# Performance work log

Measured on AMD Instinct MI355X. Metric: run time of the kernel, lower is better.

Reference implementation:

```python
import jax, jax.numpy as jnp
import numpy as np

B, H, W, DIM = 16, 64, 64, 512
GH, GW = 8, 8
NH = 16
HD = DIM // NH
POS = DIM // 16  # DynamicPosBias pos_dim = (dim//4)//4 = 32
EPS = 1e-5


def setup_inputs() -> dict:
    key = jax.random.key(0)
    ks = jax.random.split(key, 12)
    w = lambda k, s: jax.random.normal(k, s, jnp.float32) * 0.02
    f32 = jnp.float32
    return {
        "x": jax.random.normal(ks[0], (B, H * W, DIM), f32),
        "norm1_g": jnp.ones((DIM,), f32), "norm1_b": jnp.zeros((DIM,), f32),
        "qkv_w": w(ks[1], (3 * DIM, DIM)), "qkv_b": jnp.zeros((3 * DIM,), f32),
        "proj_w": w(ks[2], (DIM, DIM)), "proj_b": jnp.zeros((DIM,), f32),
        "pos_w0": w(ks[3], (POS, 2)), "pos_b0": jnp.zeros((POS,), f32),
        "pos_ln0_g": jnp.ones((POS,), f32), "pos_ln0_b": jnp.zeros((POS,), f32),
        "pos_w1": w(ks[4], (POS, POS)), "pos_b1": jnp.zeros((POS,), f32),
        "pos_ln1_g": jnp.ones((POS,), f32), "pos_ln1_b": jnp.zeros((POS,), f32),
        "pos_w2": w(ks[5], (POS, POS)), "pos_b2": jnp.zeros((POS,), f32),
        "pos_ln2_g": jnp.ones((POS,), f32), "pos_ln2_b": jnp.zeros((POS,), f32),
        "pos_w3": w(ks[6], (NH, POS)), "pos_b3": jnp.zeros((NH,), f32),
        "norm2_g": jnp.ones((DIM,), f32), "norm2_b": jnp.zeros((DIM,), f32),
        "mlp_w1": w(ks[7], (4 * DIM, DIM)), "mlp_b1": jnp.zeros((4 * DIM,), f32),
        "mlp_w2": w(ks[8], (DIM, 4 * DIM)), "mlp_b2": jnp.zeros((DIM,), f32),
    }


def _ln(x, g, b):
    m = jnp.mean(x, -1, keepdims=True)
    v = jnp.mean(jnp.square(x - m), -1, keepdims=True)
    return (x - m) * jax.lax.rsqrt(v + EPS) * g + b


def _rel_bias_tables():
    # relative coordinate table [(2GH-1)*(2GW-1), 2]
    ph = jnp.arange(1 - GH, GH)
    pw = jnp.arange(1 - GW, GW)
    biases = jnp.stack(jnp.meshgrid(ph, pw, indexing="ij")).reshape(2, -1).T.astype(jnp.float32)
    # relative position index [GH*GW, GH*GW]
    coords = jnp.stack(jnp.meshgrid(jnp.arange(GH), jnp.arange(GW), indexing="ij")).reshape(2, -1)
    rel = (coords[:, :, None] - coords[:, None, :]).transpose(1, 2, 0)  # [N,N,2]
    idx = (rel[..., 0] + GH - 1) * (2 * GW - 1) + (rel[..., 1] + GW - 1)
    return biases, idx


def reference(x, norm1_g, norm1_b, qkv_w, qkv_b, proj_w, proj_b,
              pos_w0, pos_b0, pos_ln0_g, pos_ln0_b,
              pos_w1, pos_b1, pos_ln1_g, pos_ln1_b,
              pos_w2, pos_b2, pos_ln2_g, pos_ln2_b,
              pos_w3, pos_b3, norm2_g, norm2_b,
              mlp_w1, mlp_b1, mlp_w2, mlp_b2):
    biases, rel_idx = _rel_bias_tables()
    Ng = GH * GW
    scale = HD ** -0.5

    shortcut = x
    h = _ln(x, norm1_g, norm1_b).reshape(B, H, W, DIM)
    # use_lda=True: long-distance (strided) grouping
    h = h.reshape(B, GH, H // GH, GW, W // GW, DIM).transpose(0, 2, 4, 1, 3, 5)
    h = h.reshape(B * (H * W) // Ng, Ng, DIM)  # [G, Ng, C]

    # attention
    qkv = h @ qkv_w.T + qkv_b
    qkv = qkv.reshape(-1, Ng, 3, NH, HD).transpose(2, 0, 3, 1, 4)  # [3,G,NH,Ng,HD]
    q, k, v = qkv[0], qkv[1], qkv[2]
    attn = jnp.einsum("ghnd,ghmd->ghnm", q * scale, k)

    # dynamic position bias MLP on the coordinate table
    p = jax.nn.relu(_ln(biases @ pos_w0.T + pos_b0, pos_ln0_g, pos_ln0_b))
    p = jax.nn.relu(_ln(p @ pos_w1.T + pos_b1, pos_ln1_g, pos_ln1_b))
    p = jax.nn.relu(_ln(p @ pos_w2.T + pos_b2, pos_ln2_g, pos_ln2_b))
    p = p @ pos_w3.T + pos_b3  # [(2GH-1)(2GW-1), NH]
    rel_bias = p[rel_idx].transpose(2, 0, 1)  # [NH, Ng, Ng]

    attn = jax.nn.softmax(attn + rel_bias[None], axis=-1)
    o = jnp.einsum("ghnm,ghmd->ghnd", attn, v)
    o = o.transpose(0, 2, 1, 3).reshape(-1, Ng, DIM)
    o = o @ proj_w.T + proj_b

    # ungroup (inverse of lda grouping)
    o = o.reshape(B, H // GH, W // GW, GH, GW, DIM)
    o = o.transpose(0, 3, 1, 4, 2, 5).reshape(B, H * W, DIM)

    x = shortcut + o
    m = _ln(x, norm2_g, norm2_b)
    m = jax.nn.gelu(m @ mlp_w1.T + mlp_b1, approximate=False)
    m = m @ mlp_w2.T + mlp_b2
    return x + m
```

## Files before the change

### kernel.cpp

```cpp
#include <hip/hip_runtime.h>
#include <hip/hip_bf16.h>

typedef __bf16 bf16;
typedef __bf16 bf16x8 __attribute__((ext_vector_type(8)));
typedef __bf16 bf16x4 __attribute__((ext_vector_type(4)));
typedef float f32x4_t __attribute__((ext_vector_type(4)));

static constexpr int kDIM = 512;

static constexpr size_t OFF_QKVW = 0;
static constexpr size_t OFF_PROJW = 1572864;
static constexpr size_t OFF_W1   = 2097152;
static constexpr size_t OFF_W2   = 4194304;
static constexpr size_t OFF_PTAB = 6291456;
static constexpr size_t OFF_A    = 8388608;
static constexpr size_t OFF_B    = 276824064;

typedef __attribute__((address_space(3))) uint32_t lds_u32_t;
typedef __attribute__((address_space(1))) const uint32_t glb_u32_t;
#define ASYNC_COPY16(gp, lp) __builtin_amdgcn_global_load_lds((glb_u32_t*)(gp), (lds_u32_t*)(lp), 16, 0, 0)
#define WAITV0() asm volatile("s_waitcnt vmcnt(0)" ::: "memory")

__global__ void cast_bf16_k(const float* __restrict__ in, bf16* __restrict__ out, int n4)
{
    int i = blockIdx.x * blockDim.x + threadIdx.x;
    if (i < n4) {
        float4 v = ((const float4*)in)[i];
        bf16x4 o; o[0] = (bf16)v.x; o[1] = (bf16)v.y; o[2] = (bf16)v.z; o[3] = (bf16)v.w;
        ((bf16x4*)out)[i] = o;
    }
}

__global__ void cast_fp8_k(const float* __restrict__ in, unsigned char* __restrict__ out, int n4)
{
    int i = blockIdx.x * blockDim.x + threadIdx.x;
    if (i < n4) {
        float4 v = ((const float4*)in)[i];
        int p = __builtin_amdgcn_cvt_pk_fp8_f32(v.x * 64.0f, v.y * 64.0f, 0, false);
        p = __builtin_amdgcn_cvt_pk_fp8_f32(v.z * 64.0f, v.w * 64.0f, p, true);
        ((unsigned int*)out)[i] = (unsigned int)p;
    }
}

template<int GROUP>
__global__ __launch_bounds__(256)
void ln_k(const float* __restrict__ x, const float* __restrict__ gw,
          const float* __restrict__ bw, unsigned char* __restrict__ out)
{
    const int t = blockIdx.x * 4 + (threadIdx.x >> 6);
    const int lane = threadIdx.x & 63;
    const float* xp = x + (size_t)t * kDIM + lane * 8;
    float4 p0 = *(const float4*)xp;
    float4 p1 = *(const float4*)(xp + 4);
    float v[8] = {p0.x, p0.y, p0.z, p0.w, p1.x, p1.y, p1.z, p1.w};
    float s = 0.f;
#pragma unroll
    for (int i = 0; i < 8; ++i) s += v[i];
#pragma unroll
    for (int off = 32; off > 0; off >>= 1) s += __shfl_xor(s, off);
    const float mean = s * (1.0f / 512.0f);
    float q = 0.f;
#pragma unroll
    for (int i = 0; i < 8; ++i) { float d = v[i] - mean; q += d * d; }
#pragma unroll
    for (int off = 32; off > 0; off >>= 1) q += __shfl_xor(q, off);
    const float rstd = rsqrtf(q * (1.0f / 512.0f) + 1e-5f);
    size_t orow;
    if (GROUP) {
        int b = t >> 12, r = (t >> 6) & 63, c = t & 63;
        int g = b * 64 + (r & 7) * 8 + (c & 7);
        int n = (r >> 3) * 8 + (c >> 3);
        orow = (size_t)g * 64 + n;
    } else {
        orow = t;
    }
    float4 g0 = *(const float4*)(gw + lane * 8);
    float4 g1 = *(const float4*)(gw + lane * 8 + 4);
    float4 b0 = *(const float4*)(bw + lane * 8);
    float4 b1 = *(const float4*)(bw + lane * 8 + 4);
    float gg[8] = {g0.x, g0.y, g0.z, g0.w, g1.x, g1.y, g1.z, g1.w};
    float bb[8] = {b0.x, b0.y, b0.z, b0.w, b1.x, b1.y, b1.z, b1.w};
    float o[8];
#pragma unroll
    for (int i = 0; i < 8; ++i) o[i] = ((v[i] - mean) * rstd * gg[i] + bb[i]) * 32.0f;
    unsigned int lo = 0, hi = 0;
    lo = (unsigned int)__builtin_amdgcn_cvt_pk_fp8_f32(o[0], o[1], 0, false);
    lo = (unsigned int)__builtin_amdgcn_cvt_pk_fp8_f32(o[2], o[3], (int)lo, true);
    hi = (unsigned int)__builtin_amdgcn_cvt_pk_fp8_f32(o[4], o[5], 0, false);
    hi = (unsigned int)__builtin_amdgcn_cvt_pk_fp8_f32(o[6], o[7], (int)hi, true);
    uint2 u; u.x = lo; u.y = hi;
    *(uint2*)(out + orow * kDIM + lane * 8) = u;
}

__device__ inline void ln32_relu(float* h, const float* g, const float* b)
{
    float m = 0.f;
#pragma unroll
    for (int i = 0; i < 32; ++i) m += h[i];
    m *= (1.0f / 32.0f);
    float v = 0.f;
#pragma unroll
    for (int i = 0; i < 32; ++i) { float d = h[i] - m; v += d * d; }
    v *= (1.0f / 32.0f);
    float r = rsqrtf(v + 1e-5f);
#pragma unroll
    for (int i = 0; i < 32; ++i) h[i] = fmaxf((h[i] - m) * r * g[i] + b[i], 0.f);
}

__global__ __launch_bounds__(256)
void posmlp_k(const float* __restrict__ w0, const float* __restrict__ b0,
              const float* __restrict__ g0, const float* __restrict__ bb0,
              const float* __restrict__ w1, const float* __restrict__ b1,
              const float* __restrict__ g1, const float* __restrict__ bb1,
              const float* __restrict__ w2, const float* __restrict__ b2,
              const float* __restrict__ g2, const float* __restrict__ bb2,
              const float* __restrict__ w3, const float* __restrict__ b3,
              float* __restrict__ ptab)
{
    int r = threadIdx.x;
    if (r >= 225) return;
    float in0 = (float)(r / 15) - 7.0f;
    float in1 = (float)(r % 15) - 7.0f;
    float h[32], h2[32];
#pragma unroll
    for (int o = 0; o < 32; ++o) h[o] = w0[o * 2] * in0 + w0[o * 2 + 1] * in1 + b0[o];
    ln32_relu(h, g0, bb0);
#pragma unroll
    for (int o = 0; o < 32; ++o) {
        float s = b1[o];
#pragma unroll
        for (int i = 0; i < 32; ++i) s += w1[o * 32 + i] * h[i];
        h2[o] = s;
    }
    ln32_relu(h2, g1, bb1);
#pragma unroll
    for (int o = 0; o < 32; ++o) {
        float s = b2[o];
#pragma unroll
        for (int i = 0; i < 32; ++i) s += w2[o * 32 + i] * h2[i];
        h[o] = s;
    }
    ln32_relu(h, g2, bb2);
#pragma unroll
    for (int o = 0; o < 16; ++o) {
        float s = b3[o];
#pragma unroll
        for (int i = 0; i < 32; ++i) s += w3[o * 32 + i] * h[i];
        ptab[r * 16 + o] = s;
    }
}

__global__ __launch_bounds__(256)
void attn_mfma_k(const bf16* __restrict__ qkv, const float* __restrict__ ptab,
                 bf16* __restrict__ obuf)
{
    const int g  = blockIdx.x >> 1;
    const int hb = blockIdx.x & 1;
    const int w  = threadIdx.x >> 6;
    const int lane = threadIdx.x & 63;
    const int c = lane & 15, q = lane >> 4;

    __shared__ float ptl[16][240];
    __shared__ alignas(16) bf16 pl[4][4096];
    __shared__ alignas(16) bf16 vt[4][2048];

    for (int i = threadIdx.x; i < 3600; i += 256)
        ptl[i & 15][i >> 4] = ptab[i];
    __syncthreads();

    const size_t rowb = (size_t)g * 64;
    bf16* pw = pl[w];
    char* vw = (char*)vt[w];

    for (int hh = 0; hh < 2; ++hh) {
        const int head = hb * 8 + hh * 4 + w;
        const bf16* qb = qkv + rowb * 1536 + head * 32;

        bf16x8 vrow[4];
#pragma unroll
        for (int l = 0; l < 4; ++l)
            vrow[l] = *(const bf16x8*)(qb + 1024 + (size_t)lane * 1536 + l * 8);

        bf16x8 aq[4], bk[4];
#pragma unroll
        for (int i = 0; i < 4; ++i) {
            aq[i] = *(const bf16x8*)(qb + (size_t)(i * 16 + c) * 1536 + q * 8);
            bk[i] = *(const bf16x8*)(qb + 512 + (size_t)(i * 16 + c) * 1536 + q * 8);
        }

        f32x4_t s[4][4];
#pragma unroll
        for (int i = 0; i < 4; ++i)
#pragma unroll
            for (int j = 0; j < 4; ++j)
                s[i][j] = __builtin_amdgcn_mfma_f32_16x16x32_bf16(aq[i], bk[j],
                          (f32x4_t){0.f, 0.f, 0.f, 0.f}, 0, 0, 0);

#pragma unroll
        for (int l = 0; l < 4; ++l)
#pragma unroll
            for (int j = 0; j < 8; ++j) {
                const int d = l * 8 + j;
                *(bf16*)(vw + d * 128 + ((lane * 2) ^ ((d & 7) << 4))) = vrow[l][j];
            }

        const float scale = 0.17677669529663687f;
        float inv[4][4];
#pragma unroll
        for (int i = 0; i < 4; ++i)
#pragma unroll
            for (int jj = 0; jj < 4; ++jj) {
                const int n = i * 16 + q * 4 + jj;
                const int na = n >> 3, nu = n & 7;
                float mx = -1e30f;
#pragma unroll
                for (int j = 0; j < 4; ++j) {
                    const int m = j * 16 + c;
                    const int idx = (na - (m >> 3) + 7) * 15 + (nu - (m & 7) + 7);
                    float v = s[i][j][jj] * scale + ptl[head][idx];
                    s[i][j][jj] = v;
                    mx = fmaxf(mx, v);
                }
#pragma unroll
                for (int off = 1; off < 16; off <<= 1) mx = fmaxf(mx, __shfl_xor(mx, off));
                float sum = 0.f;
#pragma unroll
                for (int j = 0; j < 4; ++j) {
                    float e = __expf(s[i][j][jj] - mx);
                    s[i][j][jj] = e; sum += e;
                }
#pragma unroll
                for (int off = 1; off < 16; off <<= 1) sum += __shfl_xor(sum, off);
                inv[i][jj] = 1.0f / sum;
            }

#pragma unroll
        for (int i = 0; i < 4; ++i)
#pragma unroll
            for (int jj = 0; jj < 4; ++jj) {
                const int n = i * 16 + q * 4 + jj;
                const int swz = (n & 7) << 4;
#pragma unroll
                for (int j = 0; j < 4; ++j) {
                    const int m = j * 16 + c;
                    *(bf16*)((char*)pw + n * 128 + ((m * 2) ^ swz)) = (bf16)s[i][j][jj];
                }
            }

        bf16x8 bv[2][2];
#pragma unroll
        for (int ks = 0; ks < 2; ++ks)
#pragma unroll
            for (int dt = 0; dt < 2; ++dt)
                bv[ks][dt] = *(const bf16x8*)(vw + (dt * 16 + c) * 128 +
                              ((ks * 64 + q * 16) ^ ((c & 7) << 4)));

        f32x4_t o[4][2];
#pragma unroll
        for (int i = 0; i < 4; ++i)
#pragma unroll
            for (int dt = 0; dt < 2; ++dt)
                o[i][dt] = (f32x4_t){0.f, 0.f, 0.f, 0.f};
#pragma unroll
        for (int ks = 0; ks < 2; ++ks)
#pragma unroll
            for (int i = 0; i < 4; ++i) {
                const int n = i * 16 + c;
                bf16x8 ap = *(const bf16x8*)((char*)pw + n * 128 +
                             ((ks * 64 + q * 16) ^ ((n & 7) << 4)));
#pragma unroll
                for (int dt = 0; dt < 2; ++dt)
                    o[i][dt] = __builtin_amdgcn_mfma_f32_16x16x32_bf16(ap, bv[ks][dt], o[i][dt], 0, 0, 0);
            }

        bf16* ob = obuf + rowb * 512 + head * 32;
#pragma unroll
        for (int i = 0; i < 4; ++i)
#pragma unroll
            for (int dt = 0; dt < 2; ++dt)
#pragma unroll
                for (int jj = 0; jj < 4; ++jj) {
                    const int n = i * 16 + q * 4 + jj;
                    ob[(size_t)n * 512 + dt * 16 + c] = (bf16)(o[i][dt][jj] * inv[i][jj]);
                }
    }
}

template<int MODE, int NBX>
__global__ __launch_bounds__(256, 2)
void gemm_bt(const bf16* __restrict__ A, const bf16* __restrict__ Bw,
             const float* __restrict__ bias, const float* __restrict__ resid,
             bf16* __restrict__ outb, float* __restrict__ outf,
             int N, int K)
{
    __shared__ alignas(16) bf16 As[128 * 64];
    __shared__ alignas(16) bf16 Bs[128 * 64];
    const int tid = threadIdx.x;
    const int lane = tid & 63;
    const int w = tid >> 6;
    const int wr = w >> 1, wc = w & 1;

    const int bid = blockIdx.y * NBX + blockIdx.x;
    const int nwg = gridDim.y * NBX;
    const int swz = (bid & 7) * (nwg >> 3) + (bid >> 3);
    const int by = swz / NBX;
    const int bx = swz - by * NBX;
    const int rowBase = by * 128;
    const int colBase = bx * 128;

    f32x4_t acc[4][4];
#pragma unroll
    for (int m = 0; m < 4; ++m)
#pragma unroll
        for (int n = 0; n < 4; ++n)
            acc[m][n] = (f32x4_t){0.f, 0.f, 0.f, 0.f};

    const int sw = (lane & 7) << 4;

    for (int kt = 0; kt < K; kt += 64) {
#pragma unroll
        for (int l = 0; l < 4; ++l) {
            const int cg = l * 256 + tid;
            const int row = cg >> 3;
            const int col8 = (cg & 7) ^ (row & 7);
            const int cu = l * 256 + (tid & 192);
            ASYNC_COPY16(A + (size_t)(rowBase + row) * K + kt + col8 * 8, As + cu * 8);
            ASYNC_COPY16(Bw + (size_t)(colBase + row) * K + kt + col8 * 8, Bs + cu * 8);
        }
        WAITV0();
        __syncthreads();
#pragma unroll
        for (int kk = 0; kk < 64; kk += 32) {
            const int bofs = kk * 2 + (lane >> 4) * 16;
            bf16x8 af[4], bfr[4];
#pragma unroll
            for (int m = 0; m < 4; ++m) {
                const int row = wr * 64 + m * 16 + (lane & 15);
                af[m] = *(const bf16x8*)((const char*)As + row * 128 + (bofs ^ sw));
            }
#pragma unroll
            for (int n = 0; n < 4; ++n) {
                const int row = wc * 64 + n * 16 + (lane & 15);
                bfr[n] = *(const bf16x8*)((const char*)Bs + row * 128 + (bofs ^ sw));
            }
#pragma unroll
            for (int m = 0; m < 4; ++m)
#pragma unroll
                for (int n = 0; n < 4; ++n)
                    acc[m][n] = __builtin_amdgcn_mfma_f32_16x16x32_bf16(af[m], bfr[n], acc[m][n], 0, 0, 0);
        }
        __syncthreads();
    }

#pragma unroll
    for (int m = 0; m < 4; ++m) {
#pragma unroll
        for (int jj = 0; jj < 4; ++jj) {
            int grow = rowBase + wr * 64 + m * 16 + (lane >> 4) * 4 + jj;
#pragma unroll
            for (int n = 0; n < 4; ++n) {
                int gcol = colBase + wc * 64 + n * 16 + (lane & 15);
                float v = acc[m][n][jj] + bias[gcol];
                if constexpr (MODE == 0) {
                    outb[(size_t)grow * N + gcol] = (bf16)v;
                } else if constexpr (MODE == 2) {
                    int g = grow >> 6, ns = grow & 63;
                    int b = g >> 6, i = (g >> 3) & 7, j = g & 7;
                    int a = ns >> 3, u = ns & 7;
                    int t = b * 4096 + (a * 8 + i) * 64 + (u * 8 + j);
                    size_t oi = (size_t)t * 512 + gcol;
                    outf[oi] = resid[oi] + v;
                }
            }
        }
    }
}

template<int MODE, int NBX>
__global__ __launch_bounds__(256, 2)
void gemm_fp8(const unsigned char* __restrict__ A, const unsigned char* __restrict__ Bw,
              const float* __restrict__ bias, const float* __restrict__ resid,
              void* __restrict__ outp, int N, int K, float invs)
{
    __shared__ alignas(16) unsigned char As[128 * 64];
    __shared__ alignas(16) unsigned char Bs[128 * 64];
    const int tid = threadIdx.x;
    const int lane = tid & 63;
    const int w = tid >> 6;
    const int wr = w >> 1, wc = w & 1;
    const int c = lane & 15, q = lane >> 4;

    const int bid = blockIdx.y * NBX + blockIdx.x;
    const int nwg = gridDim.y * NBX;
    const int swz = (bid & 7) * (nwg >> 3) + (bid >> 3);
    const int by = swz / NBX;
    const int bx = swz - by * NBX;
    const int rowBase = by * 128;
    const int colBase = bx * 128;

    f32x4_t acc[4][4];
#pragma unroll
    for (int m = 0; m < 4; ++m)
#pragma unroll
        for (int n = 0; n < 4; ++n)
            acc[m][n] = (f32x4_t){0.f, 0.f, 0.f, 0.f};

    const int f = (c >> 1) & 3;
    const int hb8 = (q & 1) * 8;

    for (int kt = 0; kt < K; kt += 64) {
#pragma unroll
        for (int l = 0; l < 2; ++l) {
            const int cg = l * 256 + tid;
            const int row = cg >> 2;
            const int sg = (cg & 3) ^ ((cg >> 3) & 3);
            const int cu = l * 256 + (tid & 192);
            ASYNC_COPY16(A + (size_t)(rowBase + row) * K + kt + sg * 16, As + cu * 16);
            ASYNC_COPY16(Bw + (size_t)(colBase + row) * K + kt + sg * 16, Bs + cu * 16);
        }
        WAITV0();
        __syncthreads();
#pragma unroll
        for (int kk = 0; kk < 64; kk += 32) {
            const int sb = (((((kk >> 4) + (q >> 1)) ^ f) << 4)) + hb8;
            long af[4], bfr[4];
#pragma unroll
            for (int m = 0; m < 4; ++m) {
                const int row = wr * 64 + m * 16 + c;
                af[m] = *(const long*)((const char*)As + row * 64 + sb);
            }
#pragma unroll
            for (int n = 0; n < 4; ++n) {
                const int row = wc * 64 + n * 16 + c;
                bfr[n] = *(const long*)((const char*)Bs + row * 64 + sb);
            }
#pragma unroll
            for (int m = 0; m < 4; ++m)
#pragma unroll
                for (int n = 0; n < 4; ++n)
                    acc[m][n] = __builtin_amdgcn_mfma_f32_16x16x32_fp8_fp8(af[m], bfr[n], acc[m][n], 0, 0, 0);
        }
        __syncthreads();
    }

#pragma unroll
    for (int m = 0; m < 4; ++m) {
#pragma unroll
        for (int jj = 0; jj < 4; ++jj) {
            int grow = rowBase + wr * 64 + m * 16 + q * 4 + jj;
#pragma unroll
            for (int n = 0; n < 4; ++n) {
                int gcol = colBase + wc * 64 + n * 16 + c;
                float v = acc[m][n][jj] * invs + bias[gcol];
                if constexpr (MODE == 0) {
                    ((bf16*)outp)[(size_t)grow * N + gcol] = (bf16)v;
                } else if constexpr (MODE == 1) {
                    float e = __expf(1.5957691216057308f * (v + 0.044715f * v * v * v));
                    v = v * (e / (1.0f + e));
                    int p8 = __builtin_amdgcn_cvt_pk_fp8_f32(v * 64.0f, v * 64.0f, 0, false);
                    ((unsigned char*)outp)[(size_t)grow * N + gcol] = (unsigned char)(p8 & 0xff);
                } else {
                    size_t oi = (size_t)grow * 512 + gcol;
                    ((float*)outp)[oi] = resid[oi] + v;
                }
            }
        }
    }
}

extern "C" void kernel_launch(void* const* d_in, const int* in_sizes, int n_in,
                              void* d_out, int out_size, void* d_ws, size_t ws_size,
                              hipStream_t stream)
{
    const float* x    = (const float*)d_in[0];
    const float* n1g  = (const float*)d_in[1];
    const float* n1b  = (const float*)d_in[2];
    const float* qkvw = (const float*)d_in[3];
    const float* qkvb = (const float*)d_in[4];
    const float* pjw  = (const float*)d_in[5];
    const float* pjb  = (const float*)d_in[6];
    const float* pw0  = (const float*)d_in[7];
    const float* pb0  = (const float*)d_in[8];
    const float* pg0  = (const float*)d_in[9];
    const float* pbb0 = (const float*)d_in[10];
    const float* pw1  = (const float*)d_in[11];
    const float* pb1  = (const float*)d_in[12];
    const float* pg1  = (const float*)d_in[13];
    const float* pbb1 = (const float*)d_in[14];
    const float* pw2  = (const float*)d_in[15];
    const float* pb2  = (const float*)d_in[16];
    const float* pg2  = (const float*)d_in[17];
    const float* pbb2 = (const float*)d_in[18];
    const float* pw3  = (const float*)d_in[19];
    const float* pb3  = (const float*)d_in[20];
    const float* n2g  = (const float*)d_in[21];
    const float* n2b  = (const float*)d_in[22];
    const float* w1   = (const float*)d_in[23];
    const float* b1   = (const float*)d_in[24];
    const float* w2   = (const float*)d_in[25];
    const float* b2   = (const float*)d_in[26];

    char* ws = (char*)d_ws;
    unsigned char* qkvw_f8 = (unsigned char*)(ws + OFF_QKVW);
    bf16* pjw_b  = (bf16*)(ws + OFF_PROJW);
    unsigned char* w1_f8 = (unsigned char*)(ws + OFF_W1);
    unsigned char* w2_f8 = (unsigned char*)(ws + OFF_W2);
    float* ptab  = (float*)(ws + OFF_PTAB);
    bf16* bufA   = (bf16*)(ws + OFF_A);
    unsigned char* bufA8 = (unsigned char*)(ws + OFF_A);
    unsigned char* bufB8 = (unsigned char*)(ws + OFF_B);
    bf16* bufBb  = (bf16*)(ws + OFF_B);
    float* xout  = (float*)d_out;

    cast_fp8_k<<<(1536 * 512 / 4 + 255) / 256, 256, 0, stream>>>(qkvw, qkvw_f8, 1536 * 512 / 4);
    cast_bf16_k<<<(512 * 512 / 4 + 255) / 256, 256, 0, stream>>>(pjw, pjw_b, 512 * 512 / 4);
    cast_fp8_k<<<(2048 * 512 / 4 + 255) / 256, 256, 0, stream>>>(w1, w1_f8, 2048 * 512 / 4);
    cast_fp8_k<<<(512 * 2048 / 4 + 255) / 256, 256, 0, stream>>>(w2, w2_f8, 512 * 2048 / 4);

    posmlp_k<<<1, 256, 0, stream>>>(pw0, pb0, pg0, pbb0, pw1, pb1, pg1, pbb1,
                                    pw2, pb2, pg2, pbb2, pw3, pb3, ptab);

    ln_k<1><<<16384, 256, 0, stream>>>(x, n1g, n1b, bufB8);

    gemm_fp8<0, 12><<<dim3(12, 512), 256, 0, stream>>>(bufB8, qkvw_f8, qkvb, nullptr,
                                                       bufA, 1536, 512, 1.0f / 2048.0f);

    attn_mfma_k<<<2048, 256, 0, stream>>>(bufA, ptab, bufBb);

    gemm_bt<2, 4><<<dim3(4, 512), 256, 0, stream>>>(bufBb, pjw_b, pjb, x, nullptr, xout, 512, 512);

    ln_k<0><<<16384, 256, 0, stream>>>(xout, n2g, n2b, bufB8);

    gemm_fp8<1, 16><<<dim3(16, 512), 256, 0, stream>>>(bufB8, w1_f8, b1, nullptr,
                                                       bufA8, 2048, 512, 1.0f / 2048.0f);

    gemm_fp8<3, 4><<<dim3(4, 512), 256, 0, stream>>>(bufA8, w2_f8, b2, xout,
                                                     xout, 512, 2048, 1.0f / 4096.0f);
}
```

Measured before the change: 736.1 us.

## Store Q/K and attention output in FP8 and run projection GEMM in FP8

The QKV GEMM epilogue now writes Q and K as scaled FP8 and V as bf16 into a packed 2048-byte row. The attention kernel computes QK^T with FP8 MFMA and rescales the scores. Attention output is written as scaled FP8, so the output projection can reuse the FP8 GEMM with a new ungroup-plus-residual mode, and the bf16 GEMM and its cast kernel are removed. This cuts memory traffic on the intermediate buffers and raises MFMA throughput, at the cost of extra quantization error in the attention scores and projection input.

New measurement: 723.5 us. Within noise of the previous version (-1.7%).

```diff
diff --git a/kernel.cpp b/kernel.cpp
--- a/kernel.cpp
+++ b/kernel.cpp
@@ -20,16 +20,6 @@
 typedef __attribute__((address_space(1))) const uint32_t glb_u32_t;
 #define ASYNC_COPY16(gp, lp) __builtin_amdgcn_global_load_lds((glb_u32_t*)(gp), (lds_u32_t*)(lp), 16, 0, 0)
 #define WAITV0() asm volatile("s_waitcnt vmcnt(0)" ::: "memory")
-
-__global__ void cast_bf16_k(const float* __restrict__ in, bf16* __restrict__ out, int n4)
-{
-    int i = blockIdx.x * blockDim.x + threadIdx.x;
-    if (i < n4) {
-        float4 v = ((const float4*)in)[i];
-        bf16x4 o; o[0] = (bf16)v.x; o[1] = (bf16)v.y; o[2] = (bf16)v.z; o[3] = (bf16)v.w;
-        ((bf16x4*)out)[i] = o;
-    }
-}
 
 __global__ void cast_fp8_k(const float* __restrict__ in, unsigned char* __restrict__ out, int n4)
 {
@@ -151,8 +141,8 @@
 }
 
 __global__ __launch_bounds__(256)
-void attn_mfma_k(const bf16* __restrict__ qkv, const float* __restrict__ ptab,
-                 bf16* __restrict__ obuf)
+void attn_mfma_k(const unsigned char* __restrict__ qkv, const float* __restrict__ ptab,
+                 unsigned char* __restrict__ obuf)
 {
     const int g  = blockIdx.x >> 1;
     const int hb = blockIdx.x & 1;
@@ -174,18 +164,19 @@
 
     for (int hh = 0; hh < 2; ++hh) {
         const int head = hb * 8 + hh * 4 + w;
-        const bf16* qb = qkv + rowb * 1536 + head * 32;
-
+        const unsigned char* qb = qkv + rowb * 2048 + head * 32;
+
+        const bf16* vbase = (const bf16*)(qb + 1024 + head * 32);
         bf16x8 vrow[4];
 #pragma unroll
         for (int l = 0; l < 4; ++l)
-            vrow[l] = *(const bf16x8*)(qb + 1024 + (size_t)lane * 1536 + l * 8);
-
-        bf16x8 aq[4], bk[4];
+            vrow[l] = *(const bf16x8*)((const bf16*)((const char*)vbase + (size_t)lane * 2048) + l * 8);
+
+        long aq[4], bk[4];
 #pragma unroll
         for (int i = 0; i < 4; ++i) {
-            aq[i] = *(const bf16x8*)(qb + (size_t)(i * 16 + c) * 1536 + q * 8);
-            bk[i] = *(const bf16x8*)(qb + 512 + (size_t)(i * 16 + c) * 1536 + q * 8);
+            aq[i] = *(const long*)(qb + (size_t)(i * 16 + c) * 2048 + q * 8);
+            bk[i] = *(const long*)(qb + 512 + (size_t)(i * 16 + c) * 2048 + q * 8);
         }
 
         f32x4_t s[4][4];
@@ -193,7 +184,7 @@
         for (int i = 0; i < 4; ++i)
 #pragma unroll
             for (int j = 0; j < 4; ++j)
-                s[i][j] = __builtin_amdgcn_mfma_f32_16x16x32_bf16(aq[i], bk[j],
+                s[i][j] = __builtin_amdgcn_mfma_f32_16x16x32_fp8_fp8(aq[i], bk[j],
                           (f32x4_t){0.f, 0.f, 0.f, 0.f}, 0, 0, 0);
 
 #pragma unroll
@@ -204,7 +195,7 @@
                 *(bf16*)(vw + d * 128 + ((lane * 2) ^ ((d & 7) << 4))) = vrow[l][j];
             }
 
-        const float scale = 0.17677669529663687f;
+        const float scale = 0.17677669529663687f / 1024.0f;
         float inv[4][4];
 #pragma unroll
         for (int i = 0; i < 4; ++i)
@@ -273,7 +264,7 @@
                     o[i][dt] = __builtin_amdgcn_mfma_f32_16x16x32_bf16(ap, bv[ks][dt], o[i][dt], 0, 0, 0);
             }
 
-        bf16* ob = obuf + rowb * 512 + head * 32;
+        unsigned char* ob = obuf + rowb * 512 + head * 32;
 #pragma unroll
         for (int i = 0; i < 4; ++i)
 #pragma unroll
@@ -281,98 +272,10 @@
 #pragma unroll
                 for (int jj = 0; jj < 4; ++jj) {
                     const int n = i * 16 + q * 4 + jj;
-                    ob[(size_t)n * 512 + dt * 16 + c] = (bf16)(o[i][dt][jj] * inv[i][jj]);
+                    float val = o[i][dt][jj] * inv[i][jj] * 32.0f;
+                    int p8 = __builtin_amdgcn_cvt_pk_fp8_f32(val, val, 0, false);
+                    ob[(size_t)n * 512 + dt * 16 + c] = (unsigned char)(p8 & 0xff);
                 }
-    }
-}
-
-template<int MODE, int NBX>
-__global__ __launch_bounds__(256, 2)
-void gemm_bt(const bf16* __restrict__ A, const bf16* __restrict__ Bw,
-             const float* __restrict__ bias, const float* __restrict__ resid,
-             bf16* __restrict__ outb, float* __restrict__ outf,
-             int N, int K)
-{
-    __shared__ alignas(16) bf16 As[128 * 64];
-    __shared__ alignas(16) bf16 Bs[128 * 64];
-    const int tid = threadIdx.x;
-    const int lane = tid & 63;
-    const int w = tid >> 6;
-    const int wr = w >> 1, wc = w & 1;
-
-    const int bid = blockIdx.y * NBX + blockIdx.x;
-    const int nwg = gridDim.y * NBX;
-    const int swz = (bid & 7) * (nwg >> 3) + (bid >> 3);
-    const int by = swz / NBX;
-    const int bx = swz - by * NBX;
-    const int rowBase = by * 128;
-    const int colBase = bx * 128;
-
-    f32x4_t acc[4][4];
-#pragma unroll
-    for (int m = 0; m < 4; ++m)
-#pragma unroll
-        for (int n = 0; n < 4; ++n)
-            acc[m][n] = (f32x4_t){0.f, 0.f, 0.f, 0.f};
-
-    const int sw = (lane & 7) << 4;
-
-    for (int kt = 0; kt < K; kt += 64) {
-#pragma unroll
-        for (int l = 0; l < 4; ++l) {
-            const int cg = l * 256 + tid;
-            const int row = cg >> 3;
-            const int col8 = (cg & 7) ^ (row & 7);
-            const int cu = l * 256 + (tid & 192);
-            ASYNC_COPY16(A + (size_t)(rowBase + row) * K + kt + col8 * 8, As + cu * 8);
-            ASYNC_COPY16(Bw + (size_t)(colBase + row) * K + kt + col8 * 8, Bs + cu * 8);
-        }
-        WAITV0();
-        __syncthreads();
-#pragma unroll
-        for (int kk = 0; kk < 64; kk += 32) {
-            const int bofs = kk * 2 + (lane >> 4) * 16;
-            bf16x8 af[4], bfr[4];
-#pragma unroll
-            for (int m = 0; m < 4; ++m) {
-                const int row = wr * 64 + m * 16 + (lane & 15);
-                af[m] = *(const bf16x8*)((const char*)As + row * 128 + (bofs ^ sw));
-            }
-#pragma unroll
-            for (int n = 0; n < 4; ++n) {
-                const int row = wc * 64 + n * 16 + (lane & 15);
-                bfr[n] = *(const bf16x8*)((const char*)Bs + row * 128 + (bofs ^ sw));
-            }
-#pragma unroll
-            for (int m = 0; m < 4; ++m)
-#pragma unroll
-                for (int n = 0; n < 4; ++n)
-                    acc[m][n] = __builtin_amdgcn_mfma_f32_16x16x32_bf16(af[m], bfr[n], acc[m][n], 0, 0, 0);
-        }
-        __syncthreads();
-    }
-
-#pragma unroll
-    for (int m = 0; m < 4; ++m) {
-#pragma unroll
-        for (int jj = 0; jj < 4; ++jj) {
-            int grow = rowBase + wr * 64 + m * 16 + (lane >> 4) * 4 + jj;
-#pragma unroll
-            for (int n = 0; n < 4; ++n) {
-                int gcol = colBase + wc * 64 + n * 16 + (lane & 15);
-                float v = acc[m][n][jj] + bias[gcol];
-                if constexpr (MODE == 0) {
-                    outb[(size_t)grow * N + gcol] = (bf16)v;
-                } else if constexpr (MODE == 2) {
-                    int g = grow >> 6, ns = grow & 63;
-                    int b = g >> 6, i = (g >> 3) & 7, j = g & 7;
-                    int a = ns >> 3, u = ns & 7;
-                    int t = b * 4096 + (a * 8 + i) * 64 + (u * 8 + j);
-                    size_t oi = (size_t)t * 512 + gcol;
-                    outf[oi] = resid[oi] + v;
-                }
-            }
-        }
     }
 }
 
@@ -453,12 +356,25 @@
                 int gcol = colBase + wc * 64 + n * 16 + c;
                 float v = acc[m][n][jj] * invs + bias[gcol];
                 if constexpr (MODE == 0) {
-                    ((bf16*)outp)[(size_t)grow * N + gcol] = (bf16)v;
+                    char* ob = (char*)outp;
+                    if (gcol < 1024) {
+                        int p8 = __builtin_amdgcn_cvt_pk_fp8_f32(v * 32.0f, v * 32.0f, 0, false);
+                        ob[(size_t)grow * 2048 + gcol] = (char)(p8 & 0xff);
+                    } else {
+                        *(bf16*)(ob + (size_t)grow * 2048 + 1024 + (size_t)(gcol - 1024) * 2) = (bf16)v;
+                    }
                 } else if constexpr (MODE == 1) {
                     float e = __expf(1.5957691216057308f * (v + 0.044715f * v * v * v));
                     v = v * (e / (1.0f + e));
                     int p8 = __builtin_amdgcn_cvt_pk_fp8_f32(v * 64.0f, v * 64.0f, 0, false);
                     ((unsigned char*)outp)[(size_t)grow * N + gcol] = (unsigned char)(p8 & 0xff);
+                } else if constexpr (MODE == 2) {
+                    int g = grow >> 6, ns = grow & 63;
+                    int b = g >> 6, i = (g >> 3) & 7, j = g & 7;
+                    int a = ns >> 3, u = ns & 7;
+                    int t = b * 4096 + (a * 8 + i) * 64 + (u * 8 + j);
+                    size_t oi = (size_t)t * 512 + gcol;
+                    ((float*)outp)[oi] = resid[oi] + v;
                 } else {
                     size_t oi = (size_t)grow * 512 + gcol;
                     ((float*)outp)[oi] = resid[oi] + v;
@@ -502,18 +418,16 @@
 
     char* ws = (char*)d_ws;
     unsigned char* qkvw_f8 = (unsigned char*)(ws + OFF_QKVW);
-    bf16* pjw_b  = (bf16*)(ws + OFF_PROJW);
+    unsigned char* pjw_f8  = (unsigned char*)(ws + OFF_PROJW);
     unsigned char* w1_f8 = (unsigned char*)(ws + OFF_W1);
     unsigned char* w2_f8 = (unsigned char*)(ws + OFF_W2);
     float* ptab  = (float*)(ws + OFF_PTAB);
-    bf16* bufA   = (bf16*)(ws + OFF_A);
     unsigned char* bufA8 = (unsigned char*)(ws + OFF_A);
     unsigned char* bufB8 = (unsigned char*)(ws + OFF_B);
-    bf16* bufBb  = (bf16*)(ws + OFF_B);
     float* xout  = (float*)d_out;
 
     cast_fp8_k<<<(1536 * 512 / 4 + 255) / 256, 256, 0, stream>>>(qkvw, qkvw_f8, 1536 * 512 / 4);
-    cast_bf16_k<<<(512 * 512 / 4 + 255) / 256, 256, 0, stream>>>(pjw, pjw_b, 512 * 512 / 4);
+    cast_fp8_k<<<(512 * 512 / 4 + 255) / 256, 256, 0, stream>>>(pjw, pjw_f8, 512 * 512 / 4);
     cast_fp8_k<<<(2048 * 512 / 4 + 255) / 256, 256, 0, stream>>>(w1, w1_f8, 2048 * 512 / 4);
     cast_fp8_k<<<(512 * 2048 / 4 + 255) / 256, 256, 0, stream>>>(w2, w2_f8, 512 * 2048 / 4);
 
@@ -523,11 +437,12 @@
     ln_k<1><<<16384, 256, 0, stream>>>(x, n1g, n1b, bufB8);
 
     gemm_fp8<0, 12><<<dim3(12, 512), 256, 0, stream>>>(bufB8, qkvw_f8, qkvb, nullptr,
-                                                       bufA, 1536, 512, 1.0f / 2048.0f);
-
-    attn_mfma_k<<<2048, 256, 0, stream>>>(bufA, ptab, bufBb);
-
-    gemm_bt<2, 4><<<dim3(4, 512), 256, 0, stream>>>(bufBb, pjw_b, pjb, x, nullptr, xout, 512, 512);
+                                                       bufA8, 1536, 512, 1.0f / 2048.0f);
+
+    attn_mfma_k<<<2048, 256, 0, stream>>>(bufA8, ptab, bufB8);
+
+    gemm_fp8<2, 4><<<dim3(4, 512), 256, 0, stream>>>(bufB8, pjw_f8, pjb, x,
+                                                     xout, 512, 512, 1.0f / 2048.0f);
 
     ln_k<0><<<16384, 256, 0, stream>>>(xout, n2g, n2b, bufB8);
 
```
